# Performance work log

Hardware: AMD Instinct MI355X
Metric: run time of the kernel (lower is better)

Reference implementation:

```python
import jax, jax.numpy as jnp
import numpy as np

B, T, C = 2, 2048, 1024
H = 16
D = C // H  # head size 64


def setup_inputs() -> dict:
    key = jax.random.key(0)
    ks = jax.random.split(key, 9)
    s = 0.02
    return {
        "x": jax.random.normal(ks[0], (B, T, C), dtype=jnp.float32),
        "Wq": jax.random.normal(ks[1], (C, C), dtype=jnp.float32) * s,
        "bq": jnp.zeros((C,), dtype=jnp.float32),
        "Wk": jax.random.normal(ks[2], (C, C), dtype=jnp.float32) * s,
        "bk": jnp.zeros((C,), dtype=jnp.float32),
        "Wv": jax.random.normal(ks[3], (C, C), dtype=jnp.float32) * s,
        "bv": jnp.zeros((C,), dtype=jnp.float32),
        "Wo": jax.random.normal(ks[4], (C, C), dtype=jnp.float32) * s,
        "bo": jnp.zeros((C,), dtype=jnp.float32),
    }


def reference(x, Wq, bq, Wk, bk, Wv, bv, Wo, bo):
    b, t, c = x.shape
    scale = 1.0 / jnp.sqrt(jnp.asarray(D, dtype=x.dtype))
    # projections (torch Linear: x @ W.T + b), then split heads -> [B,H,T,D]
    def split_heads(y):
        return y.reshape(b, t, H, D).transpose(0, 2, 1, 3)
    q = split_heads(x @ Wq.T + bq)
    k = split_heads(x @ Wk.T + bk)
    v = split_heads(x @ Wv.T + bv)
    # scores [B,H,T,T], causal mask (triu above diagonal = -inf)
    attn = jnp.einsum("bhqd,bhkd->bhqk", q, k) * scale
    causal = jnp.tril(jnp.ones((t, t), dtype=bool))  # True = keep
    attn = jnp.where(causal[None, None], attn, -jnp.inf)
    attn = jax.nn.softmax(attn, axis=-1)
    # dropout p=0.0 -> identity
    y = jnp.einsum("bhqk,bhkd->bhqd", attn, v)
    y = y.transpose(0, 2, 1, 3).reshape(b, t, c)
    return y @ Wo.T + bo
```

## Files before the change

kernel.cpp:

```cpp
#include <hip/hip_runtime.h>
#include <hip/hip_bf16.h>
#include <stdint.h>
#include <stddef.h>


typedef __bf16 bf16;
typedef __attribute__((ext_vector_type(8))) __bf16 bf16x8;
typedef __attribute__((ext_vector_type(4))) __bf16 bf16x4;
typedef __attribute__((ext_vector_type(4))) float floatx4;

#define MFMA_16x16x32(A, B, C) __builtin_amdgcn_mfma_f32_16x16x32_bf16(A, B, C, 0, 0, 0)

static constexpr int T_SEQ = 2048;
static constexpr int CDIM  = 1024;

__device__ __forceinline__ void gl2lds16(const bf16* g, bf16* l) {
  __builtin_amdgcn_global_load_lds(
      (const __attribute__((address_space(1))) uint32_t*)g,
      (__attribute__((address_space(3))) uint32_t*)l, 16, 0, 0);
}

__global__ __launch_bounds__(256) void convert_kernel(
    const float* __restrict__ x, const float* __restrict__ Wq,
    const float* __restrict__ Wk, const float* __restrict__ Wv,
    const float* __restrict__ Wo,
    bf16* __restrict__ Xb, bf16* __restrict__ Wqkvb, bf16* __restrict__ Wob) {
  size_t i = ((size_t)blockIdx.x * 256 + threadIdx.x) * 4;
  const float* src;
  bf16* dst;
  size_t off;
  if (i < 4194304) {
    src = x; dst = Xb; off = i;
  } else {
    size_t r = i - 4194304;
    int wsel = (int)(r >> 20);
    off = r & 1048575;
    src = (wsel == 0) ? Wq : (wsel == 1) ? Wk : (wsel == 2) ? Wv : Wo;
    dst = (wsel < 3) ? (Wqkvb + ((size_t)wsel << 20)) : Wob;
  }
  float4 v = *(const float4*)(src + off);
  bf16x4 o;
  o[0] = (bf16)v.x; o[1] = (bf16)v.y; o[2] = (bf16)v.z; o[3] = (bf16)v.w;
  *(bf16x4*)(dst + off) = o;
}

__device__ __forceinline__ void gemm_tile_128x128(
    const bf16* __restrict__ A, const bf16* __restrict__ B, int K,
    bf16* As, bf16* Bs, floatx4 (&acc)[4][4], int bM, int bN) {
  const int tid = threadIdx.x;
  const int w = tid >> 6, l = tid & 63;
  const int wm = w & 1, wn = w >> 1;
  const int lr = l >> 3, cl = l & 7;
  const int fr = l & 15, q4 = l >> 4;

#pragma unroll
  for (int mi = 0; mi < 4; ++mi)
#pragma unroll
    for (int ni = 0; ni < 4; ++ni)
#pragma unroll
      for (int r = 0; r < 4; ++r) acc[mi][ni][r] = 0.0f;

  for (int k0 = 0; k0 < K; k0 += 64) {
#pragma unroll
    for (int i = 0; i < 4; ++i) {
      int row = i * 32 + w * 8 + lr;
      int cg = cl ^ (row & 7);
      gl2lds16(A + (size_t)(bM * 128 + row) * K + k0 + cg * 8,
               As + row * 64 + cl * 8);
      gl2lds16(B + (size_t)(bN * 128 + row) * K + k0 + cg * 8,
               Bs + row * 64 + cl * 8);
    }
    __syncthreads();
#pragma unroll
    for (int kk = 0; kk < 2; ++kk) {
      const int cgk = kk * 4 + q4;
      bf16x8 af[4], bfr[4];
#pragma unroll
      for (int mi = 0; mi < 4; ++mi) {
        int row = wm * 64 + mi * 16 + fr;
        af[mi] = *(const bf16x8*)(As + row * 64 + (cgk ^ (row & 7)) * 8);
      }
#pragma unroll
      for (int ni = 0; ni < 4; ++ni) {
        int row = wn * 64 + ni * 16 + fr;
        bfr[ni] = *(const bf16x8*)(Bs + row * 64 + (cgk ^ (row & 7)) * 8);
      }
#pragma unroll
      for (int mi = 0; mi < 4; ++mi)
#pragma unroll
        for (int ni = 0; ni < 4; ++ni)
          acc[mi][ni] = MFMA_16x16x32(af[mi], bfr[ni], acc[mi][ni]);
    }
    __syncthreads();
  }
}

__global__ __launch_bounds__(256) void gemm_qkv(
    const bf16* __restrict__ Xb, const bf16* __restrict__ Wqkvb,
    const float* __restrict__ bq, const float* __restrict__ bk,
    const float* __restrict__ bv,
    bf16* __restrict__ Qb, bf16* __restrict__ Kb, bf16* __restrict__ Vtb) {
  __shared__ __align__(16) bf16 As[128 * 64];
  __shared__ __align__(16) bf16 Bs[128 * 64];
  floatx4 acc[4][4];
  const int bM = blockIdx.x & 31;
  const int bN = blockIdx.x >> 5;
  gemm_tile_128x128(Xb, Wqkvb, CDIM, As, Bs, acc, bM, bN);

  const int tid = threadIdx.x;
  const int w = tid >> 6, l = tid & 63;
  const int wm = w & 1, wn = w >> 1;
  const int fc = l & 15, q4 = l >> 4;
  const float QSCALE = 0.125f * 1.44269504089f;
#pragma unroll
  for (int ni = 0; ni < 4; ++ni) {
    int j = bN * 128 + wn * 64 + ni * 16 + fc;
    int seg = j >> 10;
    int jj = j & 1023;
    int h = jj >> 6, d = jj & 63;
    const float* bp = (seg == 0) ? bq : (seg == 1) ? bk : bv;
    float bias = bp[jj];
#pragma unroll
    for (int mi = 0; mi < 4; ++mi) {
#pragma unroll
      for (int r = 0; r < 4; ++r) {
        int n = bM * 128 + wm * 64 + mi * 16 + q4 * 4 + r;
        int b = n >> 11, tt = n & 2047;
        float val = acc[mi][ni][r] + bias;
        size_t bh = (size_t)(b * 16 + h);
        if (seg == 0)
          Qb[(bh * T_SEQ + tt) * 64 + d] = (bf16)(val * QSCALE);
        else if (seg == 1)
          Kb[(bh * T_SEQ + tt) * 64 + d] = (bf16)val;
        else
          Vtb[(bh * 64 + d) * T_SEQ + tt] = (bf16)val;
      }
    }
  }
}

__global__ __launch_bounds__(256) void flash_attn(
    const bf16* __restrict__ Qb, const bf16* __restrict__ Kb,
    const bf16* __restrict__ Vtb, bf16* __restrict__ Ao) {
  __shared__ __align__(16) bf16 Ks[64 * 64];
  __shared__ __align__(16) bf16 Vs[64 * 64];
  __shared__ __align__(16) bf16 Ps[4][16 * 72];

  const int bh = blockIdx.x;
  const int qt = blockIdx.y;
  const int b = bh >> 4, h = bh & 15;
  const int tid = threadIdx.x;
  const int w = tid >> 6, l = tid & 63;
  const int fc = l & 15, q4 = l >> 4;
  const int lr = l >> 3, cl = l & 7;

  const bf16* Qg = Qb + (size_t)bh * T_SEQ * 64;
  const bf16* Kg = Kb + (size_t)bh * T_SEQ * 64;
  const bf16* Vg = Vtb + (size_t)bh * 64 * T_SEQ;

  const int qrow = qt * 64 + w * 16 + fc;
  bf16x8 qf[2];
  qf[0] = *(const bf16x8*)(Qg + (size_t)qrow * 64 + q4 * 8);
  qf[1] = *(const bf16x8*)(Qg + (size_t)qrow * 64 + 32 + q4 * 8);

  bf16x8 ones;
#pragma unroll
  for (int i = 0; i < 8; ++i) ones[i] = (bf16)1.0f;

  floatx4 o[4];
  floatx4 lacc;
#pragma unroll
  for (int ds = 0; ds < 4; ++ds)
#pragma unroll
    for (int r = 0; r < 4; ++r) o[ds][r] = 0.0f;
#pragma unroll
  for (int r = 0; r < 4; ++r) lacc[r] = 0.0f;

  for (int kv = 0; kv <= qt; ++kv) {
    const int kvbase = kv * 64;
#pragma unroll
    for (int i = 0; i < 2; ++i) {
      int row = i * 32 + w * 8 + lr;
      int cg = cl ^ (row & 7);
      gl2lds16(Kg + (size_t)(kvbase + row) * 64 + cg * 8, Ks + row * 64 + cl * 8);
      gl2lds16(Vg + (size_t)row * T_SEQ + kvbase + cg * 8, Vs + row * 64 + cl * 8);
    }
    __syncthreads();

    floatx4 s[4];
#pragma unroll
    for (int ni = 0; ni < 4; ++ni)
#pragma unroll
      for (int r = 0; r < 4; ++r) s[ni][r] = 0.0f;
#pragma unroll
    for (int kk = 0; kk < 2; ++kk) {
      const int cgk = kk * 4 + q4;
#pragma unroll
      for (int ni = 0; ni < 4; ++ni) {
        int row = ni * 16 + fc;
        bf16x8 kf = *(const bf16x8*)(Ks + row * 64 + (cgk ^ (row & 7)) * 8);
        s[ni] = MFMA_16x16x32(qf[kk], kf, s[ni]);
      }
    }

    if (kv == qt) {
#pragma unroll
      for (int ni = 0; ni < 4; ++ni)
#pragma unroll
        for (int r = 0; r < 4; ++r) {
          int kc = ni * 16 + fc, qc = w * 16 + q4 * 4 + r;
          float p = (kc > qc) ? 0.0f : __builtin_amdgcn_exp2f(s[ni][r]);
          Ps[w][(q4 * 4 + r) * 72 + ni * 16 + fc] = (bf16)p;
        }
    } else {
#pragma unroll
      for (int ni = 0; ni < 4; ++ni)
#pragma unroll
        for (int r = 0; r < 4; ++r)
          Ps[w][(q4 * 4 + r) * 72 + ni * 16 + fc] =
              (bf16)__builtin_amdgcn_exp2f(s[ni][r]);
    }

#pragma unroll
    for (int kk = 0; kk < 2; ++kk) {
      bf16x8 pf = *(const bf16x8*)(&Ps[w][fc * 72 + kk * 32 + q4 * 8]);
      const int cgk = kk * 4 + q4;
#pragma unroll
      for (int ds = 0; ds < 4; ++ds) {
        int row = ds * 16 + fc;
        bf16x8 vf = *(const bf16x8*)(Vs + row * 64 + (cgk ^ (row & 7)) * 8);
        o[ds] = MFMA_16x16x32(pf, vf, o[ds]);
      }
      lacc = MFMA_16x16x32(pf, ones, lacc);
    }
    __syncthreads();
  }

  float inv[4];
#pragma unroll
  for (int r = 0; r < 4; ++r) inv[r] = __builtin_amdgcn_rcpf(lacc[r]);
#pragma unroll
  for (int ds = 0; ds < 4; ++ds)
#pragma unroll
    for (int r = 0; r < 4; ++r) {
      int tt = qt * 64 + w * 16 + q4 * 4 + r;
      int col = h * 64 + ds * 16 + fc;
      Ao[((size_t)(b * T_SEQ + tt) << 10) + col] = (bf16)(o[ds][r] * inv[r]);
    }
}

__global__ __launch_bounds__(256) void gemm_out(
    const bf16* __restrict__ Ab, const bf16* __restrict__ Wob,
    const float* __restrict__ bo, float* __restrict__ Y) {
  __shared__ __align__(16) bf16 As[128 * 64];
  __shared__ __align__(16) bf16 Bs[128 * 64];
  floatx4 acc[4][4];
  const int bM = blockIdx.x & 31;
  const int bN = blockIdx.x >> 5;
  gemm_tile_128x128(Ab, Wob, CDIM, As, Bs, acc, bM, bN);

  const int tid = threadIdx.x;
  const int w = tid >> 6, l = tid & 63;
  const int wm = w & 1, wn = w >> 1;
  const int fc = l & 15, q4 = l >> 4;
#pragma unroll
  for (int ni = 0; ni < 4; ++ni) {
    int j = bN * 128 + wn * 64 + ni * 16 + fc;
    float bias = bo[j];
#pragma unroll
    for (int mi = 0; mi < 4; ++mi)
#pragma unroll
      for (int r = 0; r < 4; ++r) {
        int n = bM * 128 + wm * 64 + mi * 16 + q4 * 4 + r;
        Y[(size_t)n * CDIM + j] = acc[mi][ni][r] + bias;
      }
  }
}

extern "C" void kernel_launch(void* const* d_in, const int* in_sizes, int n_in,
                              void* d_out, int out_size, void* d_ws, size_t ws_size,
                              hipStream_t stream) {
  const float* x  = (const float*)d_in[0];
  const float* Wq = (const float*)d_in[1];
  const float* bq = (const float*)d_in[2];
  const float* Wk = (const float*)d_in[3];
  const float* bk = (const float*)d_in[4];
  const float* Wv = (const float*)d_in[5];
  const float* bv = (const float*)d_in[6];
  const float* Wo = (const float*)d_in[7];
  const float* bo = (const float*)d_in[8];
  float* Y = (float*)d_out;

  char* ws = (char*)d_ws;
  const size_t MB = 1024 * 1024;
  bf16* Xb    = (bf16*)(ws + 0);
  bf16* Wqkvb = (bf16*)(ws + 8 * MB);
  bf16* Wob   = (bf16*)(ws + 14 * MB);
  bf16* Qb    = (bf16*)(ws + 16 * MB);
  bf16* Kb    = (bf16*)(ws + 24 * MB);
  bf16* Vtb   = (bf16*)(ws + 32 * MB);
  bf16* Ao    = Xb;

  convert_kernel<<<8192, 256, 0, stream>>>(x, Wq, Wk, Wv, Wo, Xb, Wqkvb, Wob);
  gemm_qkv<<<32 * 24, 256, 0, stream>>>(Xb, Wqkvb, bq, bk, bv, Qb, Kb, Vtb);
  flash_attn<<<dim3(32, 32), 256, 0, stream>>>(Qb, Kb, Vtb, Ao);
  gemm_out<<<32 * 8, 256, 0, stream>>>(Ao, Wob, bo, Y);
}
```

Measured before the change: 206.9 us.

## Stage QKV epilogue through LDS, double query tile in attention, shrink out-proj tile

The QKV GEMM epilogue now writes results into shared memory first, then emits coalesced 16-byte stores to Q/K and transposed V, replacing scattered 2-byte writes. Flash attention processes two 64-row query tiles per block, so each K/V tile loaded into LDS is reused twice and half as many blocks are launched. The output GEMM switches to 64x128 tiles to launch 512 blocks instead of 256 for better CU occupancy. The trade-offs are higher register pressure in attention, causal load imbalance across fewer, larger blocks, and extra LDS traffic in the epilogue.

```diff
diff --git a/kernel.cpp b/kernel.cpp
--- a/kernel.cpp
+++ b/kernel.cpp
@@ -100,8 +100,10 @@
     const float* __restrict__ bq, const float* __restrict__ bk,
     const float* __restrict__ bv,
     bf16* __restrict__ Qb, bf16* __restrict__ Kb, bf16* __restrict__ Vtb) {
-  __shared__ __align__(16) bf16 As[128 * 64];
-  __shared__ __align__(16) bf16 Bs[128 * 64];
+  __shared__ __align__(16) bf16 smem[17408];
+  bf16* As = smem;
+  bf16* Bs = smem + 8192;
+  bf16* Cs = smem;
   floatx4 acc[4][4];
   const int bM = blockIdx.x & 31;
   const int bN = blockIdx.x >> 5;
@@ -111,30 +113,51 @@
   const int w = tid >> 6, l = tid & 63;
   const int wm = w & 1, wn = w >> 1;
   const int fc = l & 15, q4 = l >> 4;
+  const int seg = bN >> 3;
   const float QSCALE = 0.125f * 1.44269504089f;
+  const float* bp = (seg == 0) ? bq : (seg == 1) ? bk : bv;
+
 #pragma unroll
   for (int ni = 0; ni < 4; ++ni) {
-    int j = bN * 128 + wn * 64 + ni * 16 + fc;
-    int seg = j >> 10;
-    int jj = j & 1023;
-    int h = jj >> 6, d = jj & 63;
-    const float* bp = (seg == 0) ? bq : (seg == 1) ? bk : bv;
-    float bias = bp[jj];
-#pragma unroll
-    for (int mi = 0; mi < 4; ++mi) {
+    int jl = wn * 64 + ni * 16 + fc;
+    float bias = bp[(bN * 128 + jl) & 1023];
+#pragma unroll
+    for (int mi = 0; mi < 4; ++mi)
 #pragma unroll
       for (int r = 0; r < 4; ++r) {
-        int n = bM * 128 + wm * 64 + mi * 16 + q4 * 4 + r;
-        int b = n >> 11, tt = n & 2047;
+        int ttl = wm * 64 + mi * 16 + q4 * 4 + r;
         float val = acc[mi][ni][r] + bias;
-        size_t bh = (size_t)(b * 16 + h);
-        if (seg == 0)
-          Qb[(bh * T_SEQ + tt) * 64 + d] = (bf16)(val * QSCALE);
-        else if (seg == 1)
-          Kb[(bh * T_SEQ + tt) * 64 + d] = (bf16)val;
-        else
-          Vtb[(bh * 64 + d) * T_SEQ + tt] = (bf16)val;
-      }
+        if (seg == 0) val *= QSCALE;
+        int addr = (seg == 2) ? jl * 136 + ttl : ttl * 136 + jl;
+        Cs[addr] = (bf16)val;
+      }
+  }
+  __syncthreads();
+
+  const int chunk = tid & 15;
+  const int rb = (tid >> 4) * 8;
+  if (seg < 2) {
+    bf16* basep = (seg == 0) ? Qb : Kb;
+#pragma unroll
+    for (int u = 0; u < 8; ++u) {
+      int maj = rb + u;
+      bf16x8 vdat = *(const bf16x8*)(Cs + maj * 136 + chunk * 8);
+      int n = bM * 128 + maj;
+      int b = n >> 11, tt = n & 2047;
+      int j = bN * 128 + chunk * 8;
+      int h = (j >> 6) & 15, d = j & 63;
+      *(bf16x8*)(basep + (((size_t)(b * 16 + h) * T_SEQ + tt) << 6) + d) = vdat;
+    }
+  } else {
+#pragma unroll
+    for (int u = 0; u < 8; ++u) {
+      int maj = rb + u;
+      bf16x8 vdat = *(const bf16x8*)(Cs + maj * 136 + chunk * 8);
+      int j = bN * 128 + maj;
+      int h = (j >> 6) & 15, d = j & 63;
+      int n0 = bM * 128 + chunk * 8;
+      int b = n0 >> 11, tt0 = n0 & 2047;
+      *(bf16x8*)(Vtb + ((size_t)(b * 16 + h) * 64 + d) * T_SEQ + tt0) = vdat;
     }
   }
 }
@@ -144,10 +167,10 @@
     const bf16* __restrict__ Vtb, bf16* __restrict__ Ao) {
   __shared__ __align__(16) bf16 Ks[64 * 64];
   __shared__ __align__(16) bf16 Vs[64 * 64];
-  __shared__ __align__(16) bf16 Ps[4][16 * 72];
+  __shared__ __align__(16) bf16 Ps[4][2][16 * 72];
 
   const int bh = blockIdx.x;
-  const int qt = blockIdx.y;
+  const int qt2 = blockIdx.y;
   const int b = bh >> 4, h = bh & 15;
   const int tid = threadIdx.x;
   const int w = tid >> 6, l = tid & 63;
@@ -157,26 +180,35 @@
   const bf16* Qg = Qb + (size_t)bh * T_SEQ * 64;
   const bf16* Kg = Kb + (size_t)bh * T_SEQ * 64;
   const bf16* Vg = Vtb + (size_t)bh * 64 * T_SEQ;
-
-  const int qrow = qt * 64 + w * 16 + fc;
-  bf16x8 qf[2];
-  qf[0] = *(const bf16x8*)(Qg + (size_t)qrow * 64 + q4 * 8);
-  qf[1] = *(const bf16x8*)(Qg + (size_t)qrow * 64 + 32 + q4 * 8);
+  const int qbase = qt2 * 128;
+
+  bf16x8 qf[2][2];
+#pragma unroll
+  for (int mi = 0; mi < 2; ++mi) {
+    const bf16* qrow = Qg + (size_t)(qbase + mi * 64 + w * 16 + fc) * 64;
+#pragma unroll
+    for (int kk = 0; kk < 2; ++kk)
+      qf[mi][kk] = *(const bf16x8*)(qrow + kk * 32 + q4 * 8);
+  }
 
   bf16x8 ones;
 #pragma unroll
   for (int i = 0; i < 8; ++i) ones[i] = (bf16)1.0f;
 
-  floatx4 o[4];
-  floatx4 lacc;
-#pragma unroll
-  for (int ds = 0; ds < 4; ++ds)
-#pragma unroll
-    for (int r = 0; r < 4; ++r) o[ds][r] = 0.0f;
-#pragma unroll
-  for (int r = 0; r < 4; ++r) lacc[r] = 0.0f;
-
-  for (int kv = 0; kv <= qt; ++kv) {
+  floatx4 o[2][4];
+  floatx4 lacc[2];
+#pragma unroll
+  for (int mi = 0; mi < 2; ++mi) {
+#pragma unroll
+    for (int ds = 0; ds < 4; ++ds)
+#pragma unroll
+      for (int r = 0; r < 4; ++r) o[mi][ds][r] = 0.0f;
+#pragma unroll
+    for (int r = 0; r < 4; ++r) lacc[mi][r] = 0.0f;
+  }
+
+  const int kvmax = 2 * qt2 + 1;
+  for (int kv = 0; kv <= kvmax; ++kv) {
     const int kvbase = kv * 64;
 #pragma unroll
     for (int i = 0; i < 2; ++i) {
@@ -187,11 +219,15 @@
     }
     __syncthreads();
 
-    floatx4 s[4];
-#pragma unroll
-    for (int ni = 0; ni < 4; ++ni)
-#pragma unroll
-      for (int r = 0; r < 4; ++r) s[ni][r] = 0.0f;
+    const bool skip0 = (kv == 2 * qt2 + 1);
+
+    floatx4 s[2][4];
+#pragma unroll
+    for (int mi = 0; mi < 2; ++mi)
+#pragma unroll
+      for (int ni = 0; ni < 4; ++ni)
+#pragma unroll
+        for (int r = 0; r < 4; ++r) s[mi][ni][r] = 0.0f;
 #pragma unroll
     for (int kk = 0; kk < 2; ++kk) {
       const int cgk = kk * 4 + q4;
@@ -199,79 +235,140 @@
       for (int ni = 0; ni < 4; ++ni) {
         int row = ni * 16 + fc;
         bf16x8 kf = *(const bf16x8*)(Ks + row * 64 + (cgk ^ (row & 7)) * 8);
-        s[ni] = MFMA_16x16x32(qf[kk], kf, s[ni]);
-      }
-    }
-
-    if (kv == qt) {
-#pragma unroll
-      for (int ni = 0; ni < 4; ++ni)
-#pragma unroll
-        for (int r = 0; r < 4; ++r) {
-          int kc = ni * 16 + fc, qc = w * 16 + q4 * 4 + r;
-          float p = (kc > qc) ? 0.0f : __builtin_amdgcn_exp2f(s[ni][r]);
-          Ps[w][(q4 * 4 + r) * 72 + ni * 16 + fc] = (bf16)p;
-        }
-    } else {
-#pragma unroll
-      for (int ni = 0; ni < 4; ++ni)
-#pragma unroll
-        for (int r = 0; r < 4; ++r)
-          Ps[w][(q4 * 4 + r) * 72 + ni * 16 + fc] =
-              (bf16)__builtin_amdgcn_exp2f(s[ni][r]);
+        if (!skip0) s[0][ni] = MFMA_16x16x32(qf[0][kk], kf, s[0][ni]);
+        s[1][ni] = MFMA_16x16x32(qf[1][kk], kf, s[1][ni]);
+      }
+    }
+
+#pragma unroll
+    for (int mi = 0; mi < 2; ++mi) {
+      if (mi == 0 && skip0) continue;
+      const bool diag = (kv == 2 * qt2 + mi);
+      if (diag) {
+        int qc = w * 16 + q4 * 4;
+#pragma unroll
+        for (int ni = 0; ni < 4; ++ni)
+#pragma unroll
+          for (int r = 0; r < 4; ++r) {
+            int kc = ni * 16 + fc;
+            float p = (kc > qc + r) ? 0.0f : __builtin_amdgcn_exp2f(s[mi][ni][r]);
+            Ps[w][mi][(q4 * 4 + r) * 72 + ni * 16 + fc] = (bf16)p;
+          }
+      } else {
+#pragma unroll
+        for (int ni = 0; ni < 4; ++ni)
+#pragma unroll
+          for (int r = 0; r < 4; ++r)
+            Ps[w][mi][(q4 * 4 + r) * 72 + ni * 16 + fc] =
+                (bf16)__builtin_amdgcn_exp2f(s[mi][ni][r]);
+      }
     }
 
 #pragma unroll
     for (int kk = 0; kk < 2; ++kk) {
-      bf16x8 pf = *(const bf16x8*)(&Ps[w][fc * 72 + kk * 32 + q4 * 8]);
       const int cgk = kk * 4 + q4;
+      bf16x8 pf0, pf1;
+      if (!skip0) pf0 = *(const bf16x8*)(&Ps[w][0][fc * 72 + kk * 32 + q4 * 8]);
+      pf1 = *(const bf16x8*)(&Ps[w][1][fc * 72 + kk * 32 + q4 * 8]);
 #pragma unroll
       for (int ds = 0; ds < 4; ++ds) {
         int row = ds * 16 + fc;
         bf16x8 vf = *(const bf16x8*)(Vs + row * 64 + (cgk ^ (row & 7)) * 8);
-        o[ds] = MFMA_16x16x32(pf, vf, o[ds]);
-      }
-      lacc = MFMA_16x16x32(pf, ones, lacc);
-    }
-    __syncthreads();
-  }
-
-  float inv[4];
-#pragma unroll
-  for (int r = 0; r < 4; ++r) inv[r] = __builtin_amdgcn_rcpf(lacc[r]);
-#pragma unroll
-  for (int ds = 0; ds < 4; ++ds)
-#pragma unroll
-    for (int r = 0; r < 4; ++r) {
-      int tt = qt * 64 + w * 16 + q4 * 4 + r;
-      int col = h * 64 + ds * 16 + fc;
-      Ao[((size_t)(b * T_SEQ + tt) << 10) + col] = (bf16)(o[ds][r] * inv[r]);
-    }
+        if (!skip0) o[0][ds] = MFMA_16x16x32(pf0, vf, o[0][ds]);
+        o[1][ds] = MFMA_16x16x32(pf1, vf, o[1][ds]);
+      }
+      if (!skip0) lacc[0] = MFMA_16x16x32(pf0, ones, lacc[0]);
+      lacc[1] = MFMA_16x16x32(pf1, ones, lacc[1]);
+    }
+    __syncthreads();
+  }
+
+#pragma unroll
+  for (int mi = 0; mi < 2; ++mi) {
+    float inv[4];
+#pragma unroll
+    for (int r = 0; r < 4; ++r) inv[r] = __builtin_amdgcn_rcpf(lacc[mi][r]);
+#pragma unroll
+    for (int ds = 0; ds < 4; ++ds)
+#pragma unroll
+      for (int r = 0; r < 4; ++r) {
+        int tt = qbase + mi * 64 + w * 16 + q4 * 4 + r;
+        int col = h * 64 + ds * 16 + fc;
+        Ao[((size_t)(b * T_SEQ + tt) << 10) + col] = (bf16)(o[mi][ds][r] * inv[r]);
+      }
+  }
 }
 
 __global__ __launch_bounds__(256) void gemm_out(
     const bf16* __restrict__ Ab, const bf16* __restrict__ Wob,
     const float* __restrict__ bo, float* __restrict__ Y) {
-  __shared__ __align__(16) bf16 As[128 * 64];
+  __shared__ __align__(16) bf16 As[64 * 64];
   __shared__ __align__(16) bf16 Bs[128 * 64];
-  floatx4 acc[4][4];
-  const int bM = blockIdx.x & 31;
-  const int bN = blockIdx.x >> 5;
-  gemm_tile_128x128(Ab, Wob, CDIM, As, Bs, acc, bM, bN);
-
+  const int bM = blockIdx.x & 63;
+  const int bN = blockIdx.x >> 6;
   const int tid = threadIdx.x;
   const int w = tid >> 6, l = tid & 63;
   const int wm = w & 1, wn = w >> 1;
-  const int fc = l & 15, q4 = l >> 4;
+  const int lr = l >> 3, cl = l & 7;
+  const int fr = l & 15, q4 = l >> 4;
+  const int fc = fr;
+
+  floatx4 acc[2][4];
+#pragma unroll
+  for (int mi = 0; mi < 2; ++mi)
+#pragma unroll
+    for (int ni = 0; ni < 4; ++ni)
+#pragma unroll
+      for (int r = 0; r < 4; ++r) acc[mi][ni][r] = 0.0f;
+
+  for (int k0 = 0; k0 < CDIM; k0 += 64) {
+#pragma unroll
+    for (int i = 0; i < 2; ++i) {
+      int row = i * 32 + w * 8 + lr;
+      int cg = cl ^ (row & 7);
+      gl2lds16(Ab + (size_t)(bM * 64 + row) * CDIM + k0 + cg * 8,
+               As + row * 64 + cl * 8);
+    }
+#pragma unroll
+    for (int i = 0; i < 4; ++i) {
+      int row = i * 32 + w * 8 + lr;
+      int cg = cl ^ (row & 7);
+      gl2lds16(Wob + (size_t)(bN * 128 + row) * CDIM + k0 + cg * 8,
+               Bs + row * 64 + cl * 8);
+    }
+    __syncthreads();
+#pragma unroll
+    for (int kk = 0; kk < 2; ++kk) {
+      const int cgk = kk * 4 + q4;
+      bf16x8 af[2], bfr[4];
+#pragma unroll
+      for (int mi = 0; mi < 2; ++mi) {
+        int row = wm * 32 + mi * 16 + fr;
+        af[mi] = *(const bf16x8*)(As + row * 64 + (cgk ^ (row & 7)) * 8);
+      }
+#pragma unroll
+      for (int ni = 0; ni < 4; ++ni) {
+        int row = wn * 64 + ni * 16 + fr;
+        bfr[ni] = *(const bf16x8*)(Bs + row * 64 + (cgk ^ (row & 7)) * 8);
+      }
+#pragma unroll
+      for (int mi = 0; mi < 2; ++mi)
+#pragma unroll
+        for (int ni = 0; ni < 4; ++ni)
+          acc[mi][ni] = MFMA_16x16x32(af[mi], bfr[ni], acc[mi][ni]);
+    }
+    __syncthreads();
+  }
+
 #pragma unroll
   for (int ni = 0; ni < 4; ++ni) {
     int j = bN * 128 + wn * 64 + ni * 16 + fc;
     float bias = bo[j];
 #pragma unroll
-    for (int mi = 0; mi < 4; ++mi)
+    for (int mi = 0; mi < 2; ++mi)
 #pragma unroll
       for (int r = 0; r < 4; ++r) {
-        int n = bM * 128 + wm * 64 + mi * 16 + q4 * 4 + r;
+        int n = bM * 64 + wm * 32 + mi * 16 + q4 * 4 + r;
         Y[(size_t)n * CDIM + j] = acc[mi][ni][r] + bias;
       }
   }
@@ -303,6 +400,6 @@
 
   convert_kernel<<<8192, 256, 0, stream>>>(x, Wq, Wk, Wv, Wo, Xb, Wqkvb, Wob);
   gemm_qkv<<<32 * 24, 256, 0, stream>>>(Xb, Wqkvb, bq, bk, bv, Qb, Kb, Vtb);
-  flash_attn<<<dim3(32, 32), 256, 0, stream>>>(Qb, Kb, Vtb, Ao);
-  gemm_out<<<32 * 8, 256, 0, stream>>>(Ao, Wob, bo, Y);
-}
+  flash_attn<<<dim3(32, 16), 256, 0, stream>>>(Qb, Kb, Vtb, Ao);
+  gemm_out<<<64 * 8, 256, 0, stream>>>(Ao, Wob, bo, Y);
+}
```

New measurement: 208.4 us. Within noise of the previous version (+0.7%).
